# Optimization experiments

Measured on AMD Instinct MI355X. Metric: run time of the kernel, lower is better.

## Reference

```python
import jax, jax.numpy as jnp
import numpy as np

D_EMBED, N_HEADS, D_HEAD = 1024, 16, 64
B, S = 2, 2048


def setup_inputs() -> dict:
    key = jax.random.key(0)
    ks = jax.random.split(key, 5)
    sc = 0.02
    return {
        "x": jax.random.normal(ks[0], (B, S, D_EMBED), dtype=jnp.float32),
        "w_q": jax.random.normal(ks[1], (D_EMBED, N_HEADS * D_HEAD), dtype=jnp.float32) * sc,
        "w_k": jax.random.normal(ks[2], (D_EMBED, N_HEADS * D_HEAD), dtype=jnp.float32) * sc,
        "w_v": jax.random.normal(ks[3], (D_EMBED, N_HEADS * D_HEAD), dtype=jnp.float32) * sc,
        "w_o": jax.random.normal(ks[4], (N_HEADS * D_HEAD, D_EMBED), dtype=jnp.float32) * sc,
    }


def reference(x, w_q, w_k, w_v, w_o):
    b, s, _ = x.shape
    # projections -> [b, h, s, d]
    def proj(w):
        return jnp.einsum('bse,ef->bsf', x, w).reshape(b, s, N_HEADS, D_HEAD).transpose(0, 2, 1, 3)
    q, k, v = proj(w_q), proj(w_k), proj(w_v)
    scores = jnp.einsum('bhqd,bhkd->bhqk', q, k) / jnp.sqrt(jnp.float32(D_HEAD))
    causal = jnp.tril(jnp.ones((s, s), dtype=bool))  # True where allowed
    scores = jnp.where(causal[None, None], scores, -jnp.inf)
    attn = jax.nn.softmax(scores, axis=-1)
    out = jnp.einsum('bhqk,bhkd->bhqd', attn, v)
    out = out.transpose(0, 2, 1, 3).reshape(b, s, N_HEADS * D_HEAD)
    return jnp.einsum('bsf,fe->bse', out, w_o)
```

## Files before the change

### kernel.cpp

```cpp
#include <hip/hip_runtime.h>
#include <hip/hip_bf16.h>
#include <cstdint>
#include <cstddef>


#define B_  2
#define S_  2048
#define E_  1024
#define NH_ 16
#define DH_ 64
#define M_  (B_*S_)
#define F_  (NH_*DH_)

typedef unsigned short u16;
typedef short short8 __attribute__((ext_vector_type(8)));
typedef float f32x4  __attribute__((ext_vector_type(4)));

#define QSCALE 0.125f

__device__ __forceinline__ u16 f2bf(float f) {
    union { float f; unsigned int i; } c; c.f = f;
    unsigned int x = c.i;
    x += 0x7fffu + ((x >> 16) & 1u);
    return (u16)(x >> 16);
}

__global__ __launch_bounds__(256)
void xconv(const float* __restrict__ x, u16* __restrict__ xb)
{
    size_t i = (size_t)blockIdx.x * 256 + threadIdx.x;
    const float4* s = (const float4*)(x + i*8);
    float4 a = s[0], b = s[1];
    short8 o;
    ((u16*)&o)[0] = f2bf(a.x); ((u16*)&o)[1] = f2bf(a.y);
    ((u16*)&o)[2] = f2bf(a.z); ((u16*)&o)[3] = f2bf(a.w);
    ((u16*)&o)[4] = f2bf(b.x); ((u16*)&o)[5] = f2bf(b.y);
    ((u16*)&o)[6] = f2bf(b.z); ((u16*)&o)[7] = f2bf(b.w);
    ((short8*)xb)[i] = o;
}

__global__ __launch_bounds__(256)
void wtrans(const float* __restrict__ W, u16* __restrict__ Wt)
{
    __shared__ u16 t[64][66];
    const int tid = threadIdx.x;
    const int n0 = blockIdx.x * 64;
    const int k0 = blockIdx.y * 64;
    {
        int kk = tid >> 2, nseg = (tid & 3) * 16;
        const float4* src = (const float4*)(W + (size_t)(k0+kk)*F_ + n0 + nseg);
        #pragma unroll
        for (int v = 0; v < 4; ++v) {
            float4 u = src[v];
            t[kk][nseg + v*4 + 0] = f2bf(u.x);
            t[kk][nseg + v*4 + 1] = f2bf(u.y);
            t[kk][nseg + v*4 + 2] = f2bf(u.z);
            t[kk][nseg + v*4 + 3] = f2bf(u.w);
        }
    }
    __syncthreads();
    {
        int nn = tid >> 2, kseg = (tid & 3) * 16;
        short8 o0, o1;
        #pragma unroll
        for (int i = 0; i < 8; ++i) ((u16*)&o0)[i] = t[kseg + i][nn];
        #pragma unroll
        for (int i = 0; i < 8; ++i) ((u16*)&o1)[i] = t[kseg + 8 + i][nn];
        u16* dst = Wt + (size_t)(n0+nn)*E_ + k0 + kseg;
        ((short8*)dst)[0] = o0;
        ((short8*)dst)[1] = o1;
    }
}

template<int MODE>
__global__ __launch_bounds__(256)
void gemm_bf16(const u16* __restrict__ A, const u16* __restrict__ Wt,
               void* __restrict__ Out0, void* __restrict__ Out1,
               void* __restrict__ Out2)
{
    __shared__ __align__(16) char lds[32768];
    char* lA = lds;
    char* lB = lds + 16384;

    const int tid  = threadIdx.x;
    const int lane = tid & 63;
    const int w    = tid >> 6;
    const int wr   = w >> 1, wc = w & 1;
    const int g    = lane >> 4;
    const int q15  = lane & 15;

    const int lin = blockIdx.x;
    const int j   = lin >> 3, xc = lin & 7;
    const int bx  = ((xc >> 2) << 2) + (j & 3);
    int by, z;
    if (MODE == 0) {
        by = ((xc & 3) << 3) + ((j >> 2) & 7);
        z  = j >> 5;
    } else {
        by = ((xc & 3) << 3) + (j >> 2);
        z  = 0;
    }

    const u16* Wz  = Wt + (size_t)z * E_ * F_;
    void*      Out = (z == 0) ? Out0 : (z == 1) ? Out1 : Out2;
    const float osc = (MODE == 0 && z == 0) ? QSCALE : 1.0f;

    const int lr  = lane >> 3;
    const int lc  = lane & 7;
    const int swz = ((lc ^ lr) << 4);

    const int b2 = by >> 4;
    const int s0 = (by & 15) * 128;

    f32x4 acc[4][4];
    #pragma unroll
    for (int i = 0; i < 4; ++i)
        #pragma unroll
        for (int jj = 0; jj < 4; ++jj) acc[i][jj] = (f32x4){0.f,0.f,0.f,0.f};

    for (int it = 0; it < E_/64; ++it) {
        const int k0 = it * 64;
        __syncthreads();
        #pragma unroll
        for (int i = 0; i < 4; ++i) {
            const int row = w*32 + i*8 + lr;
            const char* ga;
            if (MODE == 0) {
                ga = (const char*)A + (size_t)(by*128 + row)*2048 + k0*2 + swz;
            } else {
                const int h = k0 >> 6;
                ga = (const char*)A +
                     ((size_t)(b2*NH_ + h)*S_ + s0 + row)*128 + swz;
            }
            __builtin_amdgcn_global_load_lds(
                (const unsigned int*)ga,
                (unsigned int*)(lA + w*4096 + i*1024), 16, 0, 0);
        }
        #pragma unroll
        for (int i = 0; i < 4; ++i) {
            const int row = w*32 + i*8 + lr;
            const char* gb = (const char*)Wz + (size_t)(bx*128 + row)*2048
                             + k0*2 + swz;
            __builtin_amdgcn_global_load_lds(
                (const unsigned int*)gb,
                (unsigned int*)(lB + w*4096 + i*1024), 16, 0, 0);
        }
        __syncthreads();

        #pragma unroll
        for (int s = 0; s < 2; ++s) {
            short8 af[4], bfr[4];
            #pragma unroll
            for (int mt = 0; mt < 4; ++mt) {
                int row = wr*64 + mt*16 + q15;
                af[mt] = *(const short8*)(lA + row*128 + ((s*64 + 16*g) ^ ((row&7)<<4)));
            }
            #pragma unroll
            for (int nt = 0; nt < 4; ++nt) {
                int n = wc*64 + nt*16 + q15;
                bfr[nt] = *(const short8*)(lB + n*128 + ((s*64 + 16*g) ^ ((n&7)<<4)));
            }
            #pragma unroll
            for (int mt = 0; mt < 4; ++mt)
                #pragma unroll
                for (int nt = 0; nt < 4; ++nt)
                    acc[mt][nt] = __builtin_amdgcn_mfma_f32_16x16x32_bf16(
                        af[mt], bfr[nt], acc[mt][nt], 0, 0, 0);
        }
    }

    #pragma unroll
    for (int mt = 0; mt < 4; ++mt) {
        #pragma unroll
        for (int r = 0; r < 4; ++r) {
            int grow = by*128 + wr*64 + mt*16 + 4*g + r;
            if (MODE == 0) {
                int bb = grow >> 11, ss = grow & (S_-1);
                #pragma unroll
                for (int nt = 0; nt < 4; ++nt) {
                    int n = bx*128 + wc*64 + nt*16 + q15;
                    int hh = n >> 6, dd = n & 63;
                    ((u16*)Out)[(((size_t)bb*NH_ + hh)*S_ + ss)*DH_ + dd] =
                        f2bf(acc[mt][nt][r] * osc);
                }
            } else {
                #pragma unroll
                for (int nt = 0; nt < 4; ++nt) {
                    int n = bx*128 + wc*64 + nt*16 + q15;
                    ((float*)Out)[(size_t)grow * F_ + n] = acc[mt][nt][r];
                }
            }
        }
    }
}

__global__ __launch_bounds__(256)
void vtrans(const u16* __restrict__ V, u16* __restrict__ Vt)
{
    __shared__ u16 t[64][66];
    const int tid = threadIdx.x;
    const int st  = blockIdx.x;
    const int bh  = blockIdx.y;

    {
        int s = tid >> 2, dseg = (tid & 3) * 16;
        const u16* src = V + ((size_t)bh*S_ + st*64 + s)*DH_ + dseg;
        short8 a = ((const short8*)src)[0];
        short8 b = ((const short8*)src)[1];
        *(short8*)&t[s][dseg]     = a;
        *(short8*)&t[s][dseg + 8] = b;
    }
    __syncthreads();
    {
        int d = tid >> 2, sseg = (tid & 3) * 16;
        short8 o0, o1;
        #pragma unroll
        for (int i = 0; i < 8; ++i) ((u16*)&o0)[i] = t[sseg + i][d];
        #pragma unroll
        for (int i = 0; i < 8; ++i) ((u16*)&o1)[i] = t[sseg + 8 + i][d];
        u16* dst = Vt + ((size_t)bh*DH_ + d)*S_ + st*64 + sseg;
        ((short8*)dst)[0] = o0;
        ((short8*)dst)[1] = o1;
    }
}

__global__ __launch_bounds__(256)
void attn_v10(const u16* Q, const u16* __restrict__ K,
              const u16* __restrict__ Vt, u16* O)
{
    __shared__ __align__(16) char vls[2*8192];
    __shared__ __align__(16) char kls[2*8192];

    const int tid  = threadIdx.x;
    const int lane = tid & 63;
    const int w    = tid >> 6;
    const int g    = lane >> 4;
    const int q15  = lane & 15;

    const int blk = blockIdx.x;
    const int qg  = 31 - (blk >> 5);
    const int bh  = blk & 31;
    const int q0  = qg * 64;

    const u16* Kb  = K  + (size_t)bh * S_ * DH_;
    const u16* Vtb = Vt + (size_t)bh * DH_ * S_;

    short8 qf0, qf1;
    {
        const u16* Qp = Q + ((size_t)bh * S_ + q0 + w*16 + q15) * DH_ + g*8;
        qf0 = *(const short8*)(Qp);
        qf1 = *(const short8*)(Qp + 32);
    }

    f32x4 o[4];
    #pragma unroll
    for (int dt = 0; dt < 4; ++dt) o[dt] = (f32x4){0.f,0.f,0.f,0.f};
    float lrow = 0.f;

    const int sd = tid >> 2;
    const int sk = (tid & 3) * 32;

    short8 svv0, svv1, svk0, svk1;
    auto LOADX = [&](int t) {
        const u16* vs = Vtb + (size_t)sd * S_ + t*64 + (sk >> 1);
        svv0 = ((const short8*)vs)[0];
        svv1 = ((const short8*)vs)[1];
        const u16* ks = Kb + (size_t)(t*64 + sd) * DH_ + (sk >> 1);
        svk0 = ((const short8*)ks)[0];
        svk1 = ((const short8*)ks)[1];
    };
    auto WRITEX = [&](int buf) {
        char* vdst = vls + buf*8192 + sd*128;
        *(short8*)(vdst + ((sk     ) ^ ((sd&7)<<4))) = svv0;
        *(short8*)(vdst + ((sk + 16) ^ ((sd&7)<<4))) = svv1;
        char* kdst = kls + buf*8192 + sd*128;
        *(short8*)(kdst + ((sk     ) ^ ((sd&7)<<4))) = svk0;
        *(short8*)(kdst + ((sk + 16) ^ ((sd&7)<<4))) = svk1;
    };

    LOADX(0);
    WRITEX(0);
    __syncthreads();

    for (int kt = 0; ; ++kt) {
        const bool more = (kt < qg);
        if (more) LOADX(kt + 1);

        const int cur = kt & 1;
        const char* kt_ = kls + cur * 8192;
        const char* vt_ = vls + cur * 8192;
        char* plw = kls + (cur ^ 1) * 8192 + w * 2048;

        float p[16];
        __builtin_amdgcn_s_setprio(1);
        #pragma unroll
        for (int t = 0; t < 4; ++t) {
            int r = t*16 + q15;
            short8 kf0 = *(const short8*)(kt_ + r*128 + ((16*g     ) ^ ((r&7)<<4)));
            short8 kf1 = *(const short8*)(kt_ + r*128 + ((16*g + 64) ^ ((r&7)<<4)));
            f32x4 st = (f32x4){0.f,0.f,0.f,0.f};
            st = __builtin_amdgcn_mfma_f32_16x16x32_bf16(kf0, qf0, st, 0, 0, 0);
            st = __builtin_amdgcn_mfma_f32_16x16x32_bf16(kf1, qf1, st, 0, 0, 0);
            #pragma unroll
            for (int r2 = 0; r2 < 4; ++r2) p[t*4+r2] = st[r2];
        }
        __builtin_amdgcn_s_setprio(0);

        if (kt == qg) {
            #pragma unroll
            for (int t = 0; t < 4; ++t)
                #pragma unroll
                for (int r = 0; r < 4; ++r)
                    if (16*t + 4*g + r > w*16 + q15) p[t*4+r] = -1e30f;
        }

        float psum = 0.f;
        #pragma unroll
        for (int i = 0; i < 16; ++i) { p[i] = __expf(p[i]); psum += p[i]; }
        psum += __shfl_xor(psum, 16);
        psum += __shfl_xor(psum, 32);
        lrow += psum;

        #pragma unroll
        for (int t = 0; t < 4; ++t) {
            unsigned r0, r1;
            asm("v_cvt_pk_bf16_f32 %0, %1, %2"
                : "=v"(r0) : "v"(p[t*4+0]), "v"(p[t*4+1]));
            asm("v_cvt_pk_bf16_f32 %0, %1, %2"
                : "=v"(r1) : "v"(p[t*4+2]), "v"(p[t*4+3]));
            int byte = q15*128 + ((32*t + 8*g) ^ ((q15&7)<<4));
            uint2 pk; pk.x = r0; pk.y = r1;
            *(uint2*)(plw + byte) = pk;
        }

        __builtin_amdgcn_s_setprio(1);
        #pragma unroll
        for (int c = 0; c < 2; ++c) {
            int pb = q15*128 + ((64*c + 16*g) ^ ((q15&7)<<4));
            short8 pf = *(const short8*)(plw + pb);
            #pragma unroll
            for (int dt = 0; dt < 4; ++dt) {
                int d = dt*16 + q15;
                int vb = d*128 + ((64*c + 16*g) ^ ((d&7)<<4));
                short8 vf = *(const short8*)(vt_ + vb);
                o[dt] = __builtin_amdgcn_mfma_f32_16x16x32_bf16(pf, vf, o[dt], 0, 0, 0);
            }
        }
        __builtin_amdgcn_s_setprio(0);

        if (!more) break;
        WRITEX(cur ^ 1);
        __syncthreads();
    }

    float inv = 1.f / lrow;
    #pragma unroll
    for (int r = 0; r < 4; ++r) {
        float li = __shfl(inv, 4*g + r);
        int qrow = q0 + w*16 + 4*g + r;
        #pragma unroll
        for (int dt = 0; dt < 4; ++dt) {
            O[((size_t)bh * S_ + qrow) * DH_ + dt*16 + q15] = f2bf(o[dt][r] * li);
        }
    }
}

extern "C" void kernel_launch(void* const* d_in, const int* in_sizes, int n_in,
                              void* d_out, int out_size, void* d_ws, size_t ws_size,
                              hipStream_t stream) {
    (void)in_sizes; (void)n_in; (void)out_size; (void)ws_size;
    const float* x  = (const float*)d_in[0];
    const float* wq = (const float*)d_in[1];
    const float* wk = (const float*)d_in[2];
    const float* wv = (const float*)d_in[3];
    const float* wo = (const float*)d_in[4];

    u16* Qw = (u16*)d_ws;
    u16* Kw = Qw + (size_t)M_ * F_;
    u16* Vw = Kw + (size_t)M_ * F_;

    u16* D0 = (u16*)d_out;
    u16* xb = D0 + (size_t)4*1024*1024;

    xconv<<<dim3(M_*E_/8/256), 256, 0, stream>>>(x, xb);
    wtrans<<<dim3(16,16), 256, 0, stream>>>(wq, D0 + 0*(size_t)E_*F_);
    wtrans<<<dim3(16,16), 256, 0, stream>>>(wk, D0 + 1*(size_t)E_*F_);
    wtrans<<<dim3(16,16), 256, 0, stream>>>(wv, D0 + 2*(size_t)E_*F_);

    gemm_bf16<0><<<dim3(768), 256, 0, stream>>>(
        xb, D0, (void*)Qw, (void*)Kw, (void*)Vw);

    vtrans<<<dim3(S_/64, B_*NH_), 256, 0, stream>>>(Vw, D0);
    wtrans<<<dim3(16,16), 256, 0, stream>>>(wo, Vw);

    attn_v10<<<dim3(B_*NH_*(S_/64)), 256, 0, stream>>>(Qw, Kw, D0, Qw);

    gemm_bf16<2><<<dim3(256), 256, 0, stream>>>(
        Qw, Vw, d_out, d_out, d_out);
}
```

Measured before the change: 131.1 us.

## Fuse conversion/transpose prep kernels and halve output GEMM tile width

Merges the x conversion and all weight transposes (including w_o when workspace allows) into a single prep launch, removing several small kernel launches and serialization points. The output projection GEMM switches to a 128x64 tile with 512 blocks so more compute units are busy. Narrower tiles reduce per-block reuse of A and add redundant A loads.

```diff
diff --git a/kernel.cpp b/kernel.cpp
--- a/kernel.cpp
+++ b/kernel.cpp
@@ -26,17 +26,61 @@
 }
 
 __global__ __launch_bounds__(256)
-void xconv(const float* __restrict__ x, u16* __restrict__ xb)
+void prep(const float* __restrict__ x,
+          const float* __restrict__ wq, const float* __restrict__ wk,
+          const float* __restrict__ wv, const float* __restrict__ wo,
+          u16* __restrict__ xb, u16* __restrict__ Wt, u16* __restrict__ wot)
 {
-    size_t i = (size_t)blockIdx.x * 256 + threadIdx.x;
-    const float4* s = (const float4*)(x + i*8);
-    float4 a = s[0], b = s[1];
-    short8 o;
-    ((u16*)&o)[0] = f2bf(a.x); ((u16*)&o)[1] = f2bf(a.y);
-    ((u16*)&o)[2] = f2bf(a.z); ((u16*)&o)[3] = f2bf(a.w);
-    ((u16*)&o)[4] = f2bf(b.x); ((u16*)&o)[5] = f2bf(b.y);
-    ((u16*)&o)[6] = f2bf(b.z); ((u16*)&o)[7] = f2bf(b.w);
-    ((short8*)xb)[i] = o;
+    const int tid = threadIdx.x;
+    const int b   = blockIdx.x;
+    if (b < 2048) {
+        size_t i = (size_t)b * 256 + tid;
+        const float4* s = (const float4*)(x + i*8);
+        float4 a = s[0], bb = s[1];
+        short8 o;
+        ((u16*)&o)[0] = f2bf(a.x);  ((u16*)&o)[1] = f2bf(a.y);
+        ((u16*)&o)[2] = f2bf(a.z);  ((u16*)&o)[3] = f2bf(a.w);
+        ((u16*)&o)[4] = f2bf(bb.x); ((u16*)&o)[5] = f2bf(bb.y);
+        ((u16*)&o)[6] = f2bf(bb.z); ((u16*)&o)[7] = f2bf(bb.w);
+        ((short8*)xb)[i] = o;
+        return;
+    }
+    __shared__ u16 t[64][66];
+    const int wb = b - 2048;
+    const int wi = wb >> 8;
+    const int tt = wb & 255;
+    const int n0 = (tt & 15) * 64;
+    const int k0 = (tt >> 4) * 64;
+    const float* W;
+    u16* dst0;
+    if (wi < 3) { W = (wi == 0) ? wq : (wi == 1) ? wk : wv;
+                  dst0 = Wt + (size_t)wi * E_ * F_; }
+    else        { W = wo; dst0 = wot; }
+
+    {
+        int kk = tid >> 2, nseg = (tid & 3) * 16;
+        const float4* src = (const float4*)(W + (size_t)(k0+kk)*F_ + n0 + nseg);
+        #pragma unroll
+        for (int v = 0; v < 4; ++v) {
+            float4 u = src[v];
+            t[kk][nseg + v*4 + 0] = f2bf(u.x);
+            t[kk][nseg + v*4 + 1] = f2bf(u.y);
+            t[kk][nseg + v*4 + 2] = f2bf(u.z);
+            t[kk][nseg + v*4 + 3] = f2bf(u.w);
+        }
+    }
+    __syncthreads();
+    {
+        int nn = tid >> 2, kseg = (tid & 3) * 16;
+        short8 o0, o1;
+        #pragma unroll
+        for (int i = 0; i < 8; ++i) ((u16*)&o0)[i] = t[kseg + i][nn];
+        #pragma unroll
+        for (int i = 0; i < 8; ++i) ((u16*)&o1)[i] = t[kseg + 8 + i][nn];
+        u16* dst = dst0 + (size_t)(n0+nn)*E_ + k0 + kseg;
+        ((short8*)dst)[0] = o0;
+        ((short8*)dst)[1] = o1;
+    }
 }
 
 __global__ __launch_bounds__(256)
@@ -78,7 +122,9 @@
                void* __restrict__ Out0, void* __restrict__ Out1,
                void* __restrict__ Out2)
 {
-    __shared__ __align__(16) char lds[32768];
+    constexpr int NT    = (MODE == 2) ? 2 : 4;
+    constexpr int BROWS = (MODE == 2) ? 2 : 4;
+    __shared__ __align__(16) char lds[(MODE == 2) ? 24576 : 32768];
     char* lA = lds;
     char* lB = lds + 16384;
 
@@ -91,13 +137,14 @@
 
     const int lin = blockIdx.x;
     const int j   = lin >> 3, xc = lin & 7;
-    const int bx  = ((xc >> 2) << 2) + (j & 3);
-    int by, z;
+    int bx, by, z;
     if (MODE == 0) {
+        bx = ((xc >> 2) << 2) + (j & 3);
         by = ((xc & 3) << 3) + ((j >> 2) & 7);
         z  = j >> 5;
     } else {
-        by = ((xc & 3) << 3) + (j >> 2);
+        bx = ((xc >> 2) << 3) + (j & 7);
+        by = ((xc & 3) << 3) + (j >> 3);
         z  = 0;
     }
 
@@ -112,11 +159,11 @@
     const int b2 = by >> 4;
     const int s0 = (by & 15) * 128;
 
-    f32x4 acc[4][4];
+    f32x4 acc[4][NT];
     #pragma unroll
     for (int i = 0; i < 4; ++i)
         #pragma unroll
-        for (int jj = 0; jj < 4; ++jj) acc[i][jj] = (f32x4){0.f,0.f,0.f,0.f};
+        for (int jj = 0; jj < NT; ++jj) acc[i][jj] = (f32x4){0.f,0.f,0.f,0.f};
 
     for (int it = 0; it < E_/64; ++it) {
         const int k0 = it * 64;
@@ -137,33 +184,33 @@
                 (unsigned int*)(lA + w*4096 + i*1024), 16, 0, 0);
         }
         #pragma unroll
-        for (int i = 0; i < 4; ++i) {
-            const int row = w*32 + i*8 + lr;
-            const char* gb = (const char*)Wz + (size_t)(bx*128 + row)*2048
+        for (int i = 0; i < BROWS; ++i) {
+            const int row = w*(BROWS*8) + i*8 + lr;
+            const char* gb = (const char*)Wz + (size_t)(bx*(NT*32) + row)*2048
                              + k0*2 + swz;
             __builtin_amdgcn_global_load_lds(
                 (const unsigned int*)gb,
-                (unsigned int*)(lB + w*4096 + i*1024), 16, 0, 0);
+                (unsigned int*)(lB + w*(BROWS*1024) + i*1024), 16, 0, 0);
         }
         __syncthreads();
 
         #pragma unroll
         for (int s = 0; s < 2; ++s) {
-            short8 af[4], bfr[4];
+            short8 af[4], bfr[NT];
             #pragma unroll
             for (int mt = 0; mt < 4; ++mt) {
                 int row = wr*64 + mt*16 + q15;
                 af[mt] = *(const short8*)(lA + row*128 + ((s*64 + 16*g) ^ ((row&7)<<4)));
             }
             #pragma unroll
-            for (int nt = 0; nt < 4; ++nt) {
-                int n = wc*64 + nt*16 + q15;
+            for (int nt = 0; nt < NT; ++nt) {
+                int n = wc*(NT*16) + nt*16 + q15;
                 bfr[nt] = *(const short8*)(lB + n*128 + ((s*64 + 16*g) ^ ((n&7)<<4)));
             }
             #pragma unroll
             for (int mt = 0; mt < 4; ++mt)
                 #pragma unroll
-                for (int nt = 0; nt < 4; ++nt)
+                for (int nt = 0; nt < NT; ++nt)
                     acc[mt][nt] = __builtin_amdgcn_mfma_f32_16x16x32_bf16(
                         af[mt], bfr[nt], acc[mt][nt], 0, 0, 0);
         }
@@ -177,7 +224,7 @@
             if (MODE == 0) {
                 int bb = grow >> 11, ss = grow & (S_-1);
                 #pragma unroll
-                for (int nt = 0; nt < 4; ++nt) {
+                for (int nt = 0; nt < NT; ++nt) {
                     int n = bx*128 + wc*64 + nt*16 + q15;
                     int hh = n >> 6, dd = n & 63;
                     ((u16*)Out)[(((size_t)bb*NH_ + hh)*S_ + ss)*DH_ + dd] =
@@ -185,8 +232,8 @@
                 }
             } else {
                 #pragma unroll
-                for (int nt = 0; nt < 4; ++nt) {
-                    int n = bx*128 + wc*64 + nt*16 + q15;
+                for (int nt = 0; nt < NT; ++nt) {
+                    int n = bx*64 + wc*32 + nt*16 + q15;
                     ((float*)Out)[(size_t)grow * F_ + n] = acc[mt][nt][r];
                 }
             }
@@ -368,7 +415,7 @@
 extern "C" void kernel_launch(void* const* d_in, const int* in_sizes, int n_in,
                               void* d_out, int out_size, void* d_ws, size_t ws_size,
                               hipStream_t stream) {
-    (void)in_sizes; (void)n_in; (void)out_size; (void)ws_size;
+    (void)in_sizes; (void)n_in; (void)out_size;
     const float* x  = (const float*)d_in[0];
     const float* wq = (const float*)d_in[1];
     const float* wk = (const float*)d_in[2];
@@ -382,19 +429,21 @@
     u16* D0 = (u16*)d_out;
     u16* xb = D0 + (size_t)4*1024*1024;
 
-    xconv<<<dim3(M_*E_/8/256), 256, 0, stream>>>(x, xb);
-    wtrans<<<dim3(16,16), 256, 0, stream>>>(wq, D0 + 0*(size_t)E_*F_);
-    wtrans<<<dim3(16,16), 256, 0, stream>>>(wk, D0 + 1*(size_t)E_*F_);
-    wtrans<<<dim3(16,16), 256, 0, stream>>>(wv, D0 + 2*(size_t)E_*F_);
+    const bool bigws = ws_size >= ((size_t)27 << 20);
+    u16* wot = bigws ? (u16*)((char*)d_ws + ((size_t)24 << 20)) : Vw;
+
+    prep<<<dim3(bigws ? 3072 : 2816), 256, 0, stream>>>(
+        x, wq, wk, wv, wo, xb, D0, wot);
 
     gemm_bf16<0><<<dim3(768), 256, 0, stream>>>(
         xb, D0, (void*)Qw, (void*)Kw, (void*)Vw);
 
     vtrans<<<dim3(S_/64, B_*NH_), 256, 0, stream>>>(Vw, D0);
-    wtrans<<<dim3(16,16), 256, 0, stream>>>(wo, Vw);
+    if (!bigws)
+        wtrans<<<dim3(16,16), 256, 0, stream>>>(wo, Vw);
 
     attn_v10<<<dim3(B_*NH_*(S_/64)), 256, 0, stream>>>(Qw, Kw, D0, Qw);
 
-    gemm_bf16<2><<<dim3(256), 256, 0, stream>>>(
-        Qw, Vw, d_out, d_out, d_out);
-}
+    gemm_bf16<2><<<dim3(512), 256, 0, stream>>>(
+        Qw, wot, d_out, d_out, d_out);
+}
```

After: 117.0 us. 10.7% less time.
